# Kernel optimization log

Measured on AMD Instinct MI355X. Metric: run time of the kernel, lower is better.

Reference implementation:

```python
import jax, jax.numpy as jnp
import numpy as np
from jax import lax

B_COEF = np.array([0.0048243445989025905, 0.019297378395610362, 0.028946067593415543,
                   0.019297378395610362, 0.0048243445989025905], dtype=np.float32)
A_COEF = np.array([1.0, -2.369513007182038, 2.3139884144002064,
                   -1.0546654058785661, 0.18737949236818502], dtype=np.float32)


def setup_inputs() -> dict:
    key = jax.random.key(0)
    x = jax.random.normal(key, (32, 16, 32768), dtype=jnp.float32)
    return {"x": x, "b": jnp.asarray(B_COEF), "a": jnp.asarray(A_COEF)}


def _odd_ext(x, n):
    left = 2.0 * x[..., :1] - x[..., 1:n + 1][..., ::-1]
    right = 2.0 * x[..., -1:] - x[..., -(n + 1):-1][..., ::-1]
    return jnp.concatenate([left, x, right], axis=-1)


def _lfilter(x, b, a):
    # Direct form II transposed IIR, zero initial conditions.
    # x: [N, T]; b, a: [K]
    b = b / a[0]
    a = a / a[0]
    K = b.shape[0]

    def step(z, xt):  # z: [N, K-1], xt: [N]
        y = b[0] * xt + z[:, 0]
        z_shift = jnp.pad(z[:, 1:], ((0, 0), (0, 1)))
        z_new = b[1:] * xt[:, None] - a[1:] * y[:, None] + z_shift
        return z_new, y

    z0 = jnp.zeros((x.shape[0], K - 1), dtype=x.dtype)
    _, y = lax.scan(step, z0, x.T)  # y: [T, N]
    return y.T


def _filtfilt(x, b, a):
    # torchaudio-style filtfilt: forward lfilter, then backward lfilter (zero ICs).
    y = _lfilter(x, b, a)
    y = _lfilter(y[:, ::-1], b, a)[:, ::-1]
    return y


def reference(x, b, a):
    scale = jnp.max(jnp.abs(x), axis=-1, keepdims=True)
    xn = x / scale
    padlen = 3 * max(a.shape[0], b.shape[0])  # static: 15
    xe = _odd_ext(xn, padlen)                 # [B, C, T + 2*padlen]
    shp = xe.shape
    y = _filtfilt(xe.reshape(-1, shp[-1]), b, a)
    y = y.reshape(shp)[..., padlen:-padlen]
    return y * scale
```

## Files before the change

### kernel.cpp

```cpp
#include <hip/hip_runtime.h>


typedef __fp16 h2 __attribute__((ext_vector_type(2)));

constexpr int kT   = 32768;
constexpr int kP   = 15;
constexpr int kC   = 64;
constexpr int kWF  = 32;
constexpr int kNCh = kT / kC;
constexpr int kTPB = 64;

#define B0 0.0048243445989025905f
#define B1 0.019297378395610362f
#define B2 0.028946067593415543f
#define B3 0.019297378395610362f
#define B4 0.0048243445989025905f
#define NA1 2.369513007182038f
#define NA2 (-2.3139884144002064f)
#define NA3 1.0546654058785661f
#define NA4 (-0.18737949236818502f)

#define STEP(xv) do { \
    y  = fmaf(B0, (xv), z1); \
    z1 = fmaf(NA1, y, fmaf(B1, (xv), z2)); \
    z2 = fmaf(NA2, y, fmaf(B2, (xv), z3)); \
    z3 = fmaf(NA3, y, fmaf(B3, (xv), z4)); \
    z4 = fmaf(NA4, y, B4 * (xv)); \
} while (0)

#define PACK2(va, vb, DST) do { \
    STEP(va); float _t = y; \
    STEP(vb); DST = __builtin_amdgcn_cvt_pkrtz(_t, y); \
} while (0)

__global__ __launch_bounds__(kTPB, 4)
void filtfilt_kernel(const float* __restrict__ x, float* __restrict__ out) {
    const int tid   = blockIdx.x * kTPB + threadIdx.x;
    const int row   = tid >> 9;
    const int chunk = tid & (kNCh - 1);
    const bool last = (chunk == kNCh - 1);
    const float* __restrict__ xr = x + (size_t)row * kT;
    float* __restrict__ outr     = out + (size_t)row * kT;
    const int s = chunk * kC;

    h2 arc[kC / 2];
    h2 wu[14];

    float z1 = 0.f, z2 = 0.f, z3 = 0.f, z4 = 0.f, y;

    if (chunk == 0) {
        const float4* x4 = (const float4*)xr;
        float4 a0 = x4[0], a1 = x4[1], a2 = x4[2], a3 = x4[3];
        float xa[16] = {a0.x,a0.y,a0.z,a0.w, a1.x,a1.y,a1.z,a1.w,
                        a2.x,a2.y,a2.z,a2.w, a3.x,a3.y,a3.z,a3.w};
        #pragma unroll
        for (int e = 0; e < kP; ++e) {
            float xv = fmaf(2.f, xa[0], -xa[kP - e]);
            STEP(xv);
        }
    } else {
        const float4* wp = (const float4*)(xr + s - kWF);
        float4 w[8];
        #pragma unroll
        for (int i = 0; i < 8; ++i) w[i] = wp[i];
        #pragma unroll
        for (int i = 0; i < 8; ++i) {
            STEP(w[i].x); STEP(w[i].y); STEP(w[i].z); STEP(w[i].w);
        }
    }

    const float4* mp = (const float4*)(xr + s);
    float4 c0 = mp[0], c1 = mp[1], c2 = mp[2], c3 = mp[3];
    #pragma unroll
    for (int m = 0; m < 4; ++m) {
        float4 n0 = c0, n1 = c1, n2 = c2, n3 = c3;
        if (m < 3) {
            n0 = mp[4 * m + 4]; n1 = mp[4 * m + 5];
            n2 = mp[4 * m + 6]; n3 = mp[4 * m + 7];
        } else if (!last) {
            n0 = mp[16]; n1 = mp[17]; n2 = mp[18]; n3 = mp[19];
        }
        PACK2(c0.x, c0.y, arc[8 * m + 0]); PACK2(c0.z, c0.w, arc[8 * m + 1]);
        PACK2(c1.x, c1.y, arc[8 * m + 2]); PACK2(c1.z, c1.w, arc[8 * m + 3]);
        PACK2(c2.x, c2.y, arc[8 * m + 4]); PACK2(c2.z, c2.w, arc[8 * m + 5]);
        PACK2(c3.x, c3.y, arc[8 * m + 6]); PACK2(c3.z, c3.w, arc[8 * m + 7]);
        c0 = n0; c1 = n1; c2 = n2; c3 = n3;
    }

    if (!last) {
        float4 d0 = mp[20], d1 = mp[21], d2 = mp[22];
        PACK2(c0.x, c0.y, wu[0]);  PACK2(c0.z, c0.w, wu[1]);
        PACK2(c1.x, c1.y, wu[2]);  PACK2(c1.z, c1.w, wu[3]);
        PACK2(c2.x, c2.y, wu[4]);  PACK2(c2.z, c2.w, wu[5]);
        PACK2(c3.x, c3.y, wu[6]);  PACK2(c3.z, c3.w, wu[7]);
        PACK2(d0.x, d0.y, wu[8]);  PACK2(d0.z, d0.w, wu[9]);
        PACK2(d1.x, d1.y, wu[10]); PACK2(d1.z, d1.w, wu[11]);
        PACK2(d2.x, d2.y, wu[12]); PACK2(d2.z, d2.w, wu[13]);
    } else {
        const float4* e4 = (const float4*)(xr + kT - 16);
        float4 b0 = e4[0], b1 = e4[1], b2 = e4[2], b3 = e4[3];
        float xa[16] = {b0.x,b0.y,b0.z,b0.w, b1.x,b1.y,b1.z,b1.w,
                        b2.x,b2.y,b2.z,b2.w, b3.x,b3.y,b3.z,b3.w};
        float pend = 0.f;
        #pragma unroll
        for (int r = 0; r < 15; ++r) {
            float xv = fmaf(2.f, xa[15], -xa[14 - r]);
            STEP(xv);
            if ((r & 1) == 0) pend = y;
            else wu[r >> 1] = __builtin_amdgcn_cvt_pkrtz(pend, y);
        }
        wu[7] = __builtin_amdgcn_cvt_pkrtz(pend, pend);
    }

    z1 = z2 = z3 = z4 = 0.f;
    if (!last) {
        #pragma unroll
        for (int k = 13; k >= 0; --k) {
            float a = (float)wu[k].y; STEP(a);
            float b = (float)wu[k].x; STEP(b);
        }
    } else {
        { float a = (float)wu[7].x; STEP(a); }
        #pragma unroll
        for (int k = 6; k >= 0; --k) {
            float a = (float)wu[k].y; STEP(a);
            float b = (float)wu[k].x; STEP(b);
        }
    }

    float4* op = (float4*)(outr + s);
    #pragma unroll
    for (int gi = 15; gi >= 0; --gi) {
        float4 o; float v;
        v = (float)arc[2 * gi + 1].y; STEP(v); o.w = y;
        v = (float)arc[2 * gi + 1].x; STEP(v); o.z = y;
        v = (float)arc[2 * gi + 0].y; STEP(v); o.y = y;
        v = (float)arc[2 * gi + 0].x; STEP(v); o.x = y;
        op[gi] = o;
    }
}

extern "C" void kernel_launch(void* const* d_in, const int* in_sizes, int n_in,
                              void* d_out, int out_size, void* d_ws, size_t ws_size,
                              hipStream_t stream) {
    const float* x = (const float*)d_in[0];
    float* out     = (float*)d_out;
    const int rows   = in_sizes[0] / kT;
    const int blocks = rows * kNCh / kTPB;
    filtfilt_kernel<<<blocks, kTPB, 0, stream>>>(x, out);
}
```

Baseline: 131.1 us.

## Stage input and output through padded LDS for coalesced global access

Each block now cooperatively loads its span of the row (plus warm-up halo) into shared memory with coalesced float4 loads. Each thread then reads its chunk from LDS with padded addressing to avoid bank conflicts. Outputs are written back to LDS and stored to global memory in a coalesced pattern, replacing per-thread strided float4 accesses. This adds barriers and LDS use that lower occupancy, with launch bounds dropped from 4 to 2.

```diff
diff --git a/kernel.cpp b/kernel.cpp
--- a/kernel.cpp
+++ b/kernel.cpp
@@ -3,12 +3,13 @@
 
 typedef __fp16 h2 __attribute__((ext_vector_type(2)));
 
-constexpr int kT   = 32768;
-constexpr int kP   = 15;
-constexpr int kC   = 64;
-constexpr int kWF  = 32;
-constexpr int kNCh = kT / kC;
-constexpr int kTPB = 64;
+constexpr int kT    = 32768;
+constexpr int kP    = 15;
+constexpr int kC    = 64;
+constexpr int kTPB  = 64;
+constexpr int kSpan = kTPB * kC;
+constexpr int kStage = kSpan + 60;
+constexpr int kLds  = 4288;
 
 #define B0 0.0048243445989025905f
 #define B1 0.019297378395610362f
@@ -33,74 +34,79 @@
     STEP(vb); DST = __builtin_amdgcn_cvt_pkrtz(_t, y); \
 } while (0)
 
-__global__ __launch_bounds__(kTPB, 4)
+__device__ __forceinline__ int pad_addr(int m) { return m + 2 * (m >> 6); }
+
+__global__ __launch_bounds__(kTPB, 2)
 void filtfilt_kernel(const float* __restrict__ x, float* __restrict__ out) {
-    const int tid   = blockIdx.x * kTPB + threadIdx.x;
-    const int row   = tid >> 9;
-    const int chunk = tid & (kNCh - 1);
-    const bool last = (chunk == kNCh - 1);
+    __shared__ float lds[kLds];
+    const int tix = threadIdx.x;
+    const int row = blockIdx.x >> 3;
+    const int blk = blockIdx.x & 7;
+    const int s0  = blk * kSpan;
+    const bool rowfirst = (blk == 0);
+    const bool rowlast  = (blk == 7);
     const float* __restrict__ xr = x + (size_t)row * kT;
     float* __restrict__ outr     = out + (size_t)row * kT;
-    const int s = chunk * kC;
+
+    #pragma unroll
+    for (int j = 0; j < 17; ++j) {
+        const int m = 256 * j + 4 * tix;
+        if (m < kStage) {
+            int g = s0 - 32 + m;
+            g = g < 0 ? 0 : g;
+            g = g > (kT - 4) ? (kT - 4) : g;
+            const float4 v = *(const float4*)(xr + g);
+            const int a = pad_addr(m);
+            *(float2*)&lds[a]     = float2{v.x, v.y};
+            *(float2*)&lds[a + 2] = float2{v.z, v.w};
+        }
+    }
+    __syncthreads();
+
+    const int base = 66 * tix;
 
     h2 arc[kC / 2];
     h2 wu[14];
-
     float z1 = 0.f, z2 = 0.f, z3 = 0.f, z4 = 0.f, y;
 
-    if (chunk == 0) {
-        const float4* x4 = (const float4*)xr;
-        float4 a0 = x4[0], a1 = x4[1], a2 = x4[2], a3 = x4[3];
-        float xa[16] = {a0.x,a0.y,a0.z,a0.w, a1.x,a1.y,a1.z,a1.w,
-                        a2.x,a2.y,a2.z,a2.w, a3.x,a3.y,a3.z,a3.w};
+    if (rowfirst && tix == 0) {
+        float xa[16];
+        #pragma unroll
+        for (int k = 0; k < 8; ++k) {
+            float2 p = *(const float2*)&lds[32 + 2 * k];
+            xa[2 * k] = p.x; xa[2 * k + 1] = p.y;
+        }
         #pragma unroll
         for (int e = 0; e < kP; ++e) {
             float xv = fmaf(2.f, xa[0], -xa[kP - e]);
             STEP(xv);
         }
     } else {
-        const float4* wp = (const float4*)(xr + s - kWF);
-        float4 w[8];
         #pragma unroll
-        for (int i = 0; i < 8; ++i) w[i] = wp[i];
-        #pragma unroll
-        for (int i = 0; i < 8; ++i) {
-            STEP(w[i].x); STEP(w[i].y); STEP(w[i].z); STEP(w[i].w);
+        for (int k = 0; k < 32; k += 2) {
+            float2 p = *(const float2*)&lds[base + k];
+            STEP(p.x); STEP(p.y);
         }
     }
 
-    const float4* mp = (const float4*)(xr + s);
-    float4 c0 = mp[0], c1 = mp[1], c2 = mp[2], c3 = mp[3];
     #pragma unroll
-    for (int m = 0; m < 4; ++m) {
-        float4 n0 = c0, n1 = c1, n2 = c2, n3 = c3;
-        if (m < 3) {
-            n0 = mp[4 * m + 4]; n1 = mp[4 * m + 5];
-            n2 = mp[4 * m + 6]; n3 = mp[4 * m + 7];
-        } else if (!last) {
-            n0 = mp[16]; n1 = mp[17]; n2 = mp[18]; n3 = mp[19];
-        }
-        PACK2(c0.x, c0.y, arc[8 * m + 0]); PACK2(c0.z, c0.w, arc[8 * m + 1]);
-        PACK2(c1.x, c1.y, arc[8 * m + 2]); PACK2(c1.z, c1.w, arc[8 * m + 3]);
-        PACK2(c2.x, c2.y, arc[8 * m + 4]); PACK2(c2.z, c2.w, arc[8 * m + 5]);
-        PACK2(c3.x, c3.y, arc[8 * m + 6]); PACK2(c3.z, c3.w, arc[8 * m + 7]);
-        c0 = n0; c1 = n1; c2 = n2; c3 = n3;
+    for (int k = 0; k < 32; k += 2) {
+        float2 p = *(const float2*)&lds[base + 32 + k];
+        PACK2(p.x, p.y, arc[k >> 1]);
+    }
+    #pragma unroll
+    for (int k = 32; k < 64; k += 2) {
+        float2 p = *(const float2*)&lds[base + 34 + k];
+        PACK2(p.x, p.y, arc[k >> 1]);
     }
 
-    if (!last) {
-        float4 d0 = mp[20], d1 = mp[21], d2 = mp[22];
-        PACK2(c0.x, c0.y, wu[0]);  PACK2(c0.z, c0.w, wu[1]);
-        PACK2(c1.x, c1.y, wu[2]);  PACK2(c1.z, c1.w, wu[3]);
-        PACK2(c2.x, c2.y, wu[4]);  PACK2(c2.z, c2.w, wu[5]);
-        PACK2(c3.x, c3.y, wu[6]);  PACK2(c3.z, c3.w, wu[7]);
-        PACK2(d0.x, d0.y, wu[8]);  PACK2(d0.z, d0.w, wu[9]);
-        PACK2(d1.x, d1.y, wu[10]); PACK2(d1.z, d1.w, wu[11]);
-        PACK2(d2.x, d2.y, wu[12]); PACK2(d2.z, d2.w, wu[13]);
-    } else {
-        const float4* e4 = (const float4*)(xr + kT - 16);
-        float4 b0 = e4[0], b1 = e4[1], b2 = e4[2], b3 = e4[3];
-        float xa[16] = {b0.x,b0.y,b0.z,b0.w, b1.x,b1.y,b1.z,b1.w,
-                        b2.x,b2.y,b2.z,b2.w, b3.x,b3.y,b3.z,b3.w};
+    if (rowlast && tix == 63) {
+        float xa[16];
+        #pragma unroll
+        for (int k = 0; k < 8; ++k) {
+            float2 p = *(const float2*)&lds[4240 + 2 * k];
+            xa[2 * k] = p.x; xa[2 * k + 1] = p.y;
+        }
         float pend = 0.f;
         #pragma unroll
         for (int r = 0; r < 15; ++r) {
@@ -110,33 +116,45 @@
             else wu[r >> 1] = __builtin_amdgcn_cvt_pkrtz(pend, y);
         }
         wu[7] = __builtin_amdgcn_cvt_pkrtz(pend, pend);
+    } else {
+        #pragma unroll
+        for (int k = 0; k < 28; k += 2) {
+            float2 p = *(const float2*)&lds[base + 98 + k];
+            PACK2(p.x, p.y, wu[k >> 1]);
+        }
     }
+    __syncthreads();
 
     z1 = z2 = z3 = z4 = 0.f;
-    if (!last) {
-        #pragma unroll
-        for (int k = 13; k >= 0; --k) {
-            float a = (float)wu[k].y; STEP(a);
-            float b = (float)wu[k].x; STEP(b);
-        }
-    } else {
+    if (rowlast && tix == 63) {
         { float a = (float)wu[7].x; STEP(a); }
         #pragma unroll
         for (int k = 6; k >= 0; --k) {
             float a = (float)wu[k].y; STEP(a);
             float b = (float)wu[k].x; STEP(b);
         }
+    } else {
+        #pragma unroll
+        for (int k = 13; k >= 0; --k) {
+            float a = (float)wu[k].y; STEP(a);
+            float b = (float)wu[k].x; STEP(b);
+        }
     }
 
-    float4* op = (float4*)(outr + s);
     #pragma unroll
-    for (int gi = 15; gi >= 0; --gi) {
-        float4 o; float v;
-        v = (float)arc[2 * gi + 1].y; STEP(v); o.w = y;
-        v = (float)arc[2 * gi + 1].x; STEP(v); o.z = y;
-        v = (float)arc[2 * gi + 0].y; STEP(v); o.y = y;
-        v = (float)arc[2 * gi + 0].x; STEP(v); o.x = y;
-        op[gi] = o;
+    for (int k = 62; k >= 0; k -= 2) {
+        float v1 = (float)arc[k >> 1].y; STEP(v1); float oy = y;
+        float v0 = (float)arc[k >> 1].x; STEP(v0);
+        *(float2*)&lds[base + k] = float2{y, oy};
+    }
+    __syncthreads();
+
+    #pragma unroll
+    for (int j2 = 0; j2 < 32; ++j2) {
+        const int q = 128 * j2 + 2 * tix;
+        const int a = 66 * (q >> 6) + (q & 63);
+        float2 p = *(const float2*)&lds[a];
+        *(float2*)(outr + s0 + q) = p;
     }
 }
 
@@ -146,6 +164,6 @@
     const float* x = (const float*)d_in[0];
     float* out     = (float*)d_out;
     const int rows   = in_sizes[0] / kT;
-    const int blocks = rows * kNCh / kTPB;
+    const int blocks = rows * 8;
     filtfilt_kernel<<<blocks, kTPB, 0, stream>>>(x, out);
 }
```

Result: slower. 134.6 us (+2.6%).
